# Optimization experiments

Hardware: AMD Instinct MI355X
Metric: run time of the kernel (lower is better)

The kernel has to match this reference:

```python
import jax, jax.numpy as jnp
import numpy as np

N_EMBD = 1024
HEAD_SIZE = 64  # n_embd // n_head = 1024 // 16


def setup_inputs() -> dict:
    key = jax.random.key(0)
    ks = jax.random.split(key, 7)
    s = 0.02
    return {
        "x": jax.random.normal(ks[0], (8, 2048, N_EMBD), dtype=jnp.float32),
        "wq": jax.random.normal(ks[1], (N_EMBD, HEAD_SIZE), dtype=jnp.float32) * s,
        "bq": jax.random.normal(ks[2], (HEAD_SIZE,), dtype=jnp.float32) * s,
        "wk": jax.random.normal(ks[3], (N_EMBD, HEAD_SIZE), dtype=jnp.float32) * s,
        "bk": jax.random.normal(ks[4], (HEAD_SIZE,), dtype=jnp.float32) * s,
        "wv": jax.random.normal(ks[5], (N_EMBD, HEAD_SIZE), dtype=jnp.float32) * s,
        "bv": jax.random.normal(ks[6], (HEAD_SIZE,), dtype=jnp.float32) * s,
    }


def reference(x, wq, bq, wk, bk, wv, bv):
    B, T, C = x.shape
    q = x @ wq + bq  # [B,T,H]
    k = x @ wk + bk
    v = x @ wv + bv
    # NOTE: original scales by C**-0.5 where C = n_embd (full embedding dim)
    scale = jnp.asarray(C, x.dtype) ** -0.5
    att = jnp.einsum("bqh,bkh->bqk", q, k) * scale  # [B,T,T]
    causal = jnp.tril(jnp.ones((T, T), dtype=bool))
    att = jnp.where(causal, att, -jnp.inf)
    att = jax.nn.softmax(att, axis=-1)
    return jnp.einsum("bqk,bkh->bqh", att, v)  # [B,T,H]
```

## Files before the change

### kernel.cpp

```cpp
#include <hip/hip_runtime.h>
#include <hip/hip_bf16.h>

typedef short s8v __attribute__((ext_vector_type(8)));
typedef short s4v __attribute__((ext_vector_type(4)));
typedef float f4v __attribute__((ext_vector_type(4)));

#define MFMA16(a,b,c) __builtin_amdgcn_mfma_f32_16x16x32_bf16((a),(b),(c),0,0,0)

__device__ __forceinline__ short f2bf(float f) {
    __hip_bfloat16 h = __float2bfloat16(f);
    short s; __builtin_memcpy(&s, &h, 2); return s;
}
__device__ __forceinline__ float bf2f(short s) {
    unsigned int u = ((unsigned int)(unsigned short)s) << 16;
    float f; __builtin_memcpy(&f, &u, 4); return f;
}
__device__ __forceinline__ s4v cvt4(float4 a) {
    s4v r; r[0] = f2bf(a.x); r[1] = f2bf(a.y); r[2] = f2bf(a.z); r[3] = f2bf(a.w);
    return r;
}

__global__ __launch_bounds__(256) void pack_w_kernel(
    const float* __restrict__ wq, const float* __restrict__ wk,
    const float* __restrict__ wv, short* __restrict__ wpack)
{
    int fid  = blockIdx.x * 256 + threadIdx.x;
    int lane = fid & 63;
    int ks   = (fid >> 6) & 31;
    int t    = fid >> 11;
    int m3 = t >> 2, nt = t & 3;
    int col = nt * 16 + (lane & 15);
    int k0  = ks * 32 + (lane >> 4) * 8;
    const float* w = (m3 == 0) ? wq : (m3 == 1 ? wk : wv);
    float sc = (m3 == 0) ? 0.03125f : 1.0f;
    s8v frag;
#pragma unroll
    for (int j = 0; j < 8; j++) frag[j] = f2bf(w[(k0 + j) * 64 + col] * sc);
    ((s8v*)wpack)[fid] = frag;
}

__global__ __launch_bounds__(512) void qkv_kernel(
    const float* __restrict__ x, const short* __restrict__ wpack,
    const float* __restrict__ bq, const float* __restrict__ bk,
    const float* __restrict__ bv,
    short* __restrict__ qws, short* __restrict__ kws, short* __restrict__ vt)
{
    __shared__ short xl[2][64][72];

    int tid  = threadIdx.x;
    int wave = tid >> 6, lane = tid & 63;
    int quad = lane >> 4, l16 = lane & 15;
    int row0 = blockIdx.x * 64;
    int rhalf = (wave & 1) * 32;
    int tbase = (wave >> 1) * 3;
    const float* xbase = x + (size_t)row0 * 1024;
    const s8v* wp = (const s8v*)wpack;

    f4v acc[2][3];
    f4v z = {0.f, 0.f, 0.f, 0.f};
#pragma unroll
    for (int rf = 0; rf < 2; rf++)
#pragma unroll
        for (int i = 0; i < 3; i++) acc[rf][i] = z;

    float4 xr[2];
#pragma unroll
    for (int i = 0; i < 2; i++) {
        int idx = i * 512 + tid;
        xr[i] = *(const float4*)(xbase + (size_t)(idx >> 4) * 1024 + (idx & 15) * 4);
    }
#pragma unroll
    for (int i = 0; i < 2; i++) {
        int idx = i * 512 + tid;
        *(s4v*)&xl[0][idx >> 4][(idx & 15) * 4] = cvt4(xr[i]);
    }
    __syncthreads();

    for (int sk = 0; sk < 16; sk++) {
        int cur = sk & 1, nxt = cur ^ 1;
        if (sk < 15) {
#pragma unroll
            for (int i = 0; i < 2; i++) {
                int idx = i * 512 + tid;
                xr[i] = *(const float4*)(xbase + (size_t)(idx >> 4) * 1024
                                         + (sk + 1) * 64 + (idx & 15) * 4);
            }
        }
#pragma unroll
        for (int ks = 0; ks < 2; ks++) {
            s8v a0 = *(const s8v*)&xl[cur][rhalf + l16][ks * 32 + quad * 8];
            s8v a1 = *(const s8v*)&xl[cur][rhalf + 16 + l16][ks * 32 + quad * 8];
            int kg = sk * 2 + ks;
#pragma unroll
            for (int i = 0; i < 3; i++) {
                s8v bf = wp[((tbase + i) * 32 + kg) * 64 + lane];
                acc[0][i] = MFMA16(a0, bf, acc[0][i]);
                acc[1][i] = MFMA16(a1, bf, acc[1][i]);
            }
        }
        if (sk < 15) {
#pragma unroll
            for (int i = 0; i < 2; i++) {
                int idx = i * 512 + tid;
                *(s4v*)&xl[nxt][idx >> 4][(idx & 15) * 4] = cvt4(xr[i]);
            }
            __syncthreads();
        }
    }

    int b = row0 >> 11;
#pragma unroll
    for (int rf = 0; rf < 2; rf++) {
        int rowD = row0 + rhalf + rf * 16 + quad * 4;
#pragma unroll
        for (int i = 0; i < 3; i++) {
            int t = tbase + i, m3 = t >> 2, nt = t & 3;
            int col = nt * 16 + l16;
            if (m3 == 0) {
                float bias = bq[col] * 0.03125f;
#pragma unroll
                for (int r = 0; r < 4; r++)
                    qws[(rowD + r) * 64 + col] = f2bf(acc[rf][i][r] + bias);
            } else if (m3 == 1) {
                float bias = bk[col];
#pragma unroll
                for (int r = 0; r < 4; r++)
                    kws[(rowD + r) * 64 + col] = f2bf(acc[rf][i][r] + bias);
            } else {
                float bias = bv[col];
                int keyb = rowD & 2047;
                s4v v4;
#pragma unroll
                for (int r = 0; r < 4; r++) v4[r] = f2bf(acc[rf][i][r] + bias);
                *(s4v*)(vt + (size_t)(b * 64 + col) * 2048 + keyb) = v4;
            }
        }
    }
}

__global__ __launch_bounds__(256) void attn_kernel(
    const short* __restrict__ qws, const short* __restrict__ kws,
    const short* __restrict__ vt, short* __restrict__ opart,
    float* __restrict__ lpart)
{
    __shared__ short Kl[2][64][72];
    __shared__ short Vl[2][64][72];
    __shared__ short Pl[4][16 * 72];

    int tid  = threadIdx.x;
    int wave = tid >> 6, lane = tid & 63;
    int quad = lane >> 4, l16 = lane & 15;
    int b = blockIdx.y;
    int u = 143 - blockIdx.x;

    int g = 0;
#pragma unroll
    for (int gg = 1; gg <= 7; gg++) if (u >= 2 * gg * (gg + 1)) g = gg;
    int rem = u - 2 * g * (g + 1);
    int qt = 4 * g + rem / (g + 1);
    int cc = rem % (g + 1);

    int q0 = qt * 64;
    int c0 = cc * 256;
    bool last = (cc == g);
    int jtN = last ? (((q0 + 63 - c0) >> 6) + 1) : 4;

    const short* qb  = qws + (size_t)b * 2048 * 64;
    const short* kb  = kws + (size_t)b * 2048 * 64;
    const short* vtb = vt  + (size_t)b * 64 * 2048;

    int qrow = q0 + wave * 16 + l16;
    s8v qf0 = *(const s8v*)(qb + qrow * 64 + quad * 8);
    s8v qf1 = *(const s8v*)(qb + qrow * 64 + 32 + quad * 8);

    s8v onef;
#pragma unroll
    for (int j = 0; j < 8; j++) onef[j] = (l16 == 0) ? (short)0x3F80 : (short)0;

    f4v o[5];
    f4v z = {0.f, 0.f, 0.f, 0.f};
#pragma unroll
    for (int nt = 0; nt < 5; nt++) o[nt] = z;

    int srow = tid >> 3;
    int sc   = (tid & 7) * 8;

    s8v kr[2], vr[2];
#pragma unroll
    for (int i = 0; i < 2; i++) {
        int r = srow + i * 32;
        kr[i] = *(const s8v*)(kb + (c0 + r) * 64 + sc);
        vr[i] = *(const s8v*)(vtb + (size_t)r * 2048 + c0 + sc);
    }
#pragma unroll
    for (int i = 0; i < 2; i++) {
        int r = srow + i * 32;
        *(s8v*)&Kl[0][r][sc] = kr[i];
        *(s8v*)&Vl[0][r][sc] = vr[i];
    }
    __syncthreads();

    for (int t = 0; t < jtN; t++) {
        int cur = t & 1, nxt = cur ^ 1;
        int key0 = c0 + t * 64;
        bool more = (t + 1 < jtN);

        if (more) {
            int key1 = key0 + 64;
#pragma unroll
            for (int i = 0; i < 2; i++) {
                int r = srow + i * 32;
                kr[i] = *(const s8v*)(kb + (key1 + r) * 64 + sc);
                vr[i] = *(const s8v*)(vtb + (size_t)r * 2048 + key1 + sc);
            }
        }

        f4v s[4];
#pragma unroll
        for (int nt = 0; nt < 4; nt++) {
            s8v k0 = *(const s8v*)&Kl[cur][nt * 16 + l16][quad * 8];
            s8v k1 = *(const s8v*)&Kl[cur][nt * 16 + l16][32 + quad * 8];
            s[nt] = MFMA16(qf0, k0, z);
            s[nt] = MFMA16(qf1, k1, s[nt]);
        }

        if (last) {
            int rowbase = q0 + wave * 16 + quad * 4;
#pragma unroll
            for (int nt = 0; nt < 4; nt++) {
                int key = key0 + nt * 16 + l16;
#pragma unroll
                for (int r = 0; r < 4; r++)
                    if (key > rowbase + r) s[nt][r] = -1e30f;
            }
        }

        short* pw = Pl[wave];
#pragma unroll
        for (int nt = 0; nt < 4; nt++)
#pragma unroll
            for (int r = 0; r < 4; r++)
                pw[(quad * 4 + r) * 72 + nt * 16 + l16] = f2bf(__expf(s[nt][r]));
        asm volatile("s_waitcnt lgkmcnt(0)" ::: "memory");

#pragma unroll
        for (int st = 0; st < 2; st++) {
            s8v pf = *(const s8v*)(pw + l16 * 72 + st * 32 + quad * 8);
#pragma unroll
            for (int nt = 0; nt < 4; nt++) {
                s8v vf = *(const s8v*)&Vl[cur][nt * 16 + l16][st * 32 + quad * 8];
                o[nt] = MFMA16(pf, vf, o[nt]);
            }
            o[4] = MFMA16(pf, onef, o[4]);
        }

        if (more) {
#pragma unroll
            for (int i = 0; i < 2; i++) {
                int r = srow + i * 32;
                *(s8v*)&Kl[nxt][r][sc] = kr[i];
                *(s8v*)&Vl[nxt][r][sc] = vr[i];
            }
            __syncthreads();
        }
    }

    int g0 = b * 2048 + q0 + wave * 16;
    short* op = opart + (size_t)cc * (16384 * 64);
#pragma unroll
    for (int nt = 0; nt < 4; nt++)
#pragma unroll
        for (int r = 0; r < 4; r++)
            op[(size_t)(g0 + quad * 4 + r) * 64 + nt * 16 + l16] = f2bf(o[nt][r]);
    if (l16 == 0) {
        float* lp = lpart + (size_t)cc * 16384;
#pragma unroll
        for (int r = 0; r < 4; r++) lp[g0 + quad * 4 + r] = o[4][r];
    }
}

__global__ __launch_bounds__(256) void combine_kernel(
    const short* __restrict__ opart, const float* __restrict__ lpart,
    float* __restrict__ out)
{
    int idx = blockIdx.x * 256 + threadIdx.x;
    int g = idx >> 4;
    int d = (idx & 15) * 4;
    int nc = ((g & 2047) >> 8) + 1;
    float s0 = 0.f, s1 = 0.f, s2 = 0.f, s3 = 0.f, lsum = 0.f;
    for (int c = 0; c < nc; c++) {
        short4 o4 = *(const short4*)(opart + (size_t)c * (16384 * 64) + g * 64 + d);
        s0 += bf2f(o4.x); s1 += bf2f(o4.y); s2 += bf2f(o4.z); s3 += bf2f(o4.w);
        lsum += lpart[c * 16384 + g];
    }
    float inv = 1.0f / lsum;
    float4 res = {s0 * inv, s1 * inv, s2 * inv, s3 * inv};
    *(float4*)(out + g * 64 + d) = res;
}

extern "C" void kernel_launch(void* const* d_in, const int* in_sizes, int n_in,
                              void* d_out, int out_size, void* d_ws, size_t ws_size,
                              hipStream_t stream) {
    const float* x  = (const float*)d_in[0];
    const float* wq = (const float*)d_in[1];
    const float* bq = (const float*)d_in[2];
    const float* wk = (const float*)d_in[3];
    const float* bk = (const float*)d_in[4];
    const float* wv = (const float*)d_in[5];
    const float* bv = (const float*)d_in[6];
    float* out = (float*)d_out;

    char* ws = (char*)d_ws;
    short* wpack = (short*)ws;
    short* qws   = (short*)(ws + (512u << 10));
    short* kws   = (short*)(ws + (512u << 10) + (2u << 20));
    short* vt    = (short*)(ws + (512u << 10) + (4u << 20));
    short* opart = (short*)(ws + (512u << 10) + (6u << 20));
    float* lpart = (float*)(ws + (512u << 10) + (22u << 20));

    hipLaunchKernelGGL(pack_w_kernel,  dim3(96),        dim3(256), 0, stream,
                       wq, wk, wv, wpack);
    hipLaunchKernelGGL(qkv_kernel,     dim3(256),       dim3(512), 0, stream,
                       x, wpack, bq, bk, bv, qws, kws, vt);
    hipLaunchKernelGGL(attn_kernel,    dim3(144, 8),    dim3(256), 0, stream,
                       qws, kws, vt, opart, lpart);
    hipLaunchKernelGGL(combine_kernel, dim3(1024),      dim3(256), 0, stream,
                       opart, lpart, out);
}
```

Before: 143.0 us.

## Transpose QK MFMA output for packed P stores and single-buffer K/V LDS

Swaps the MFMA operand order for S = K·Q so each lane holds four consecutive keys of one query row. The exp'd P values can then be packed into a single 8-byte LDS store per tile instead of four 2-byte scattered stores, and the causal mask indexing is updated to match. K/V shared memory is reduced from double-buffered to single-buffered, with two barriers per iteration around the LDS write. Register prefetch of the next tile is kept. This cuts LDS footprint, which may allow more resident blocks, but adds a barrier and exposes the LDS store latency inside each iteration.

Result: faster. 139.5 us (-2.5%).

```diff
diff --git a/kernel.cpp b/kernel.cpp
--- a/kernel.cpp
+++ b/kernel.cpp
@@ -18,6 +18,10 @@
 __device__ __forceinline__ s4v cvt4(float4 a) {
     s4v r; r[0] = f2bf(a.x); r[1] = f2bf(a.y); r[2] = f2bf(a.z); r[3] = f2bf(a.w);
     return r;
+}
+__device__ __forceinline__ unsigned int pk2(float a, float b) {
+    return ((unsigned int)(unsigned short)f2bf(b) << 16) |
+           (unsigned int)(unsigned short)f2bf(a);
 }
 
 __global__ __launch_bounds__(256) void pack_w_kernel(
@@ -143,8 +147,8 @@
     const short* __restrict__ vt, short* __restrict__ opart,
     float* __restrict__ lpart)
 {
-    __shared__ short Kl[2][64][72];
-    __shared__ short Vl[2][64][72];
+    __shared__ short Kl[64][72];
+    __shared__ short Vl[64][72];
     __shared__ short Pl[4][16 * 72];
 
     int tid  = threadIdx.x;
@@ -192,18 +196,19 @@
         kr[i] = *(const s8v*)(kb + (c0 + r) * 64 + sc);
         vr[i] = *(const s8v*)(vtb + (size_t)r * 2048 + c0 + sc);
     }
-#pragma unroll
-    for (int i = 0; i < 2; i++) {
-        int r = srow + i * 32;
-        *(s8v*)&Kl[0][r][sc] = kr[i];
-        *(s8v*)&Vl[0][r][sc] = vr[i];
-    }
-    __syncthreads();
 
     for (int t = 0; t < jtN; t++) {
-        int cur = t & 1, nxt = cur ^ 1;
         int key0 = c0 + t * 64;
         bool more = (t + 1 < jtN);
+
+        __syncthreads();
+#pragma unroll
+        for (int i = 0; i < 2; i++) {
+            int r = srow + i * 32;
+            *(s8v*)&Kl[r][sc] = kr[i];
+            *(s8v*)&Vl[r][sc] = vr[i];
+        }
+        __syncthreads();
 
         if (more) {
             int key1 = key0 + 64;
@@ -218,29 +223,31 @@
         f4v s[4];
 #pragma unroll
         for (int nt = 0; nt < 4; nt++) {
-            s8v k0 = *(const s8v*)&Kl[cur][nt * 16 + l16][quad * 8];
-            s8v k1 = *(const s8v*)&Kl[cur][nt * 16 + l16][32 + quad * 8];
-            s[nt] = MFMA16(qf0, k0, z);
-            s[nt] = MFMA16(qf1, k1, s[nt]);
+            s8v k0 = *(const s8v*)&Kl[nt * 16 + l16][quad * 8];
+            s8v k1 = *(const s8v*)&Kl[nt * 16 + l16][32 + quad * 8];
+            s[nt] = MFMA16(k0, qf0, z);
+            s[nt] = MFMA16(k1, qf1, s[nt]);
         }
 
         if (last) {
-            int rowbase = q0 + wave * 16 + quad * 4;
+            int qg = q0 + wave * 16 + l16;
 #pragma unroll
             for (int nt = 0; nt < 4; nt++) {
-                int key = key0 + nt * 16 + l16;
+                int keyb = key0 + nt * 16 + quad * 4;
 #pragma unroll
                 for (int r = 0; r < 4; r++)
-                    if (key > rowbase + r) s[nt][r] = -1e30f;
+                    if (keyb + r > qg) s[nt][r] = -1e30f;
             }
         }
 
         short* pw = Pl[wave];
 #pragma unroll
-        for (int nt = 0; nt < 4; nt++)
-#pragma unroll
-            for (int r = 0; r < 4; r++)
-                pw[(quad * 4 + r) * 72 + nt * 16 + l16] = f2bf(__expf(s[nt][r]));
+        for (int nt = 0; nt < 4; nt++) {
+            uint2 d;
+            d.x = pk2(__expf(s[nt][0]), __expf(s[nt][1]));
+            d.y = pk2(__expf(s[nt][2]), __expf(s[nt][3]));
+            *(uint2*)&pw[l16 * 72 + nt * 16 + quad * 4] = d;
+        }
         asm volatile("s_waitcnt lgkmcnt(0)" ::: "memory");
 
 #pragma unroll
@@ -248,20 +255,10 @@
             s8v pf = *(const s8v*)(pw + l16 * 72 + st * 32 + quad * 8);
 #pragma unroll
             for (int nt = 0; nt < 4; nt++) {
-                s8v vf = *(const s8v*)&Vl[cur][nt * 16 + l16][st * 32 + quad * 8];
+                s8v vf = *(const s8v*)&Vl[nt * 16 + l16][st * 32 + quad * 8];
                 o[nt] = MFMA16(pf, vf, o[nt]);
             }
             o[4] = MFMA16(pf, onef, o[4]);
-        }
-
-        if (more) {
-#pragma unroll
-            for (int i = 0; i < 2; i++) {
-                int r = srow + i * 32;
-                *(s8v*)&Kl[nxt][r][sc] = kr[i];
-                *(s8v*)&Vl[nxt][r][sc] = vr[i];
-            }
-            __syncthreads();
         }
     }
 
```
